# Performance work log

Measured on AMD Instinct MI355X. Metric: run time of the kernel, lower is better.

## Reference

```python
import jax, jax.numpy as jnp
import numpy as np

B, S, D, UNITS = 32, 4096, 512, 512


def setup_inputs() -> dict:
    key = jax.random.key(0)
    ks = jax.random.split(key, 8)
    scale = 0.05
    return {
        "query": jax.random.normal(ks[0], (B, D), dtype=jnp.float32),
        "values": jax.random.normal(ks[1], (B, S, D), dtype=jnp.float32),
        "W1": jax.random.normal(ks[2], (D, UNITS), dtype=jnp.float32) * scale,
        "b1": jnp.zeros((UNITS,), dtype=jnp.float32),
        "W2": jax.random.normal(ks[3], (D, UNITS), dtype=jnp.float32) * scale,
        "b2": jnp.zeros((UNITS,), dtype=jnp.float32),
        "V": jax.random.normal(ks[4], (UNITS, 1), dtype=jnp.float32) * scale,
        "bv": jnp.zeros((1,), dtype=jnp.float32),
    }


def reference(query, values, W1, b1, W2, b2, V, bv):
    # values: [B, S, D], query: [B, D]
    proj_v = jnp.einsum("bsd,du->bsu", values, W1) + b1          # [B, S, U]
    proj_q = (query @ W2 + b2)[:, None, :]                        # [B, 1, U]
    score = jnp.tanh(proj_v + proj_q) @ V + bv                    # [B, S, 1]
    attention_weights = jax.nn.softmax(score, axis=1)             # [B, S, 1]
    context_vector = jnp.sum(attention_weights * values, axis=1)  # [B, D]
    return (context_vector, attention_weights)
```

## Files before the change

### kernel.cpp

```cpp
#include <hip/hip_runtime.h>

#define NB 32
#define NS 4096
#define ND 512
#define NU 512

typedef __attribute__((ext_vector_type(8))) __bf16 bf16x8;
typedef __attribute__((ext_vector_type(8))) short short8;
typedef __attribute__((ext_vector_type(4))) float f32x4;

union Cvt8 { __bf16 h[8]; short8 s8; };

__device__ __forceinline__ float fast_tanh(float x) {
  float e = __expf(2.0f * x);
  return 1.0f - __fdividef(2.0f, e + 1.0f);
}

__global__ void pack_w1_kernel(const float* __restrict__ W1, __bf16* __restrict__ W1f) {
  int idx = blockIdx.x * 256 + threadIdx.x;
  int l  = idx & 63;
  int ct = (idx >> 6) & 31;
  int ks = idx >> 11;
  int col   = ct * 16 + (l & 15);
  int kbase = ks * 32 + (l >> 4) * 8;
  Cvt8 u;
#pragma unroll
  for (int j = 0; j < 8; ++j) u.h[j] = (__bf16)W1[(size_t)(kbase + j) * NU + col];
  *reinterpret_cast<short8*>(W1f + (size_t)idx * 8) = u.s8;
}

__global__ void proj_query_kernel(const float* __restrict__ query, const float* __restrict__ W2,
                                  const float* __restrict__ b2, const float* __restrict__ b1,
                                  float* __restrict__ pq) {
  int b = blockIdx.y;
  int u = blockIdx.x * 256 + threadIdx.x;
  const float* q = query + (size_t)b * ND;
  float acc = b2[u] + b1[u];
  for (int k = 0; k < ND; ++k) acc += q[k] * W2[(size_t)k * NU + u];
  pq[(size_t)b * NU + u] = acc;
}

__global__ __launch_bounds__(512, 4)
void score_kernel(const float* __restrict__ values, const __bf16* __restrict__ W1f,
                  const float* __restrict__ pq, const float* __restrict__ V,
                  float* __restrict__ scoreW) {
  __shared__ __align__(16) char ldsb[67584];
  float* sbuf = (float*)(ldsb + 65536);

  int bid = blockIdx.x;
  int b = bid >> 6;
  int s0 = (bid & 63) * 64;
  int tid = threadIdx.x;
  int l = tid & 63;
  int w = tid >> 6;
  int lane_col = l & 15;
  int lane_k8  = l >> 4;

  float pqv[4], Vv[4];
#pragma unroll
  for (int nb = 0; nb < 2; ++nb)
#pragma unroll
    for (int cf = 0; cf < 2; ++cf) {
      int col = nb * 256 + w * 32 + cf * 16 + lane_col;
      pqv[nb * 2 + cf] = pq[(size_t)b * NU + col];
      Vv[nb * 2 + cf]  = V[col];
    }

  const float* vbase = values + ((size_t)b * NS + s0) * ND;

#pragma unroll
  for (int i = 0; i < 8; ++i) {
    int c  = i * 512 + tid;
    int t  = c >> 10;
    int kg = (c >> 6) & 15;
    int ln = c & 63;
    int s  = t * 16 + (ln & 15);
    int c8 = kg * 4 + (ln >> 4);
    const float4* p = reinterpret_cast<const float4*>(vbase + (size_t)s * ND + c8 * 8);
    float4 f0 = p[0], f1 = p[1];
    Cvt8 u;
    u.h[0] = (__bf16)f0.x; u.h[1] = (__bf16)f0.y; u.h[2] = (__bf16)f0.z; u.h[3] = (__bf16)f0.w;
    u.h[4] = (__bf16)f1.x; u.h[5] = (__bf16)f1.y; u.h[6] = (__bf16)f1.z; u.h[7] = (__bf16)f1.w;
    *reinterpret_cast<short8*>(ldsb + (size_t)c * 16) = u.s8;
  }
  __syncthreads();

  float partial[4][4];
#pragma unroll
  for (int t = 0; t < 4; ++t)
#pragma unroll
    for (int r = 0; r < 4; ++r) partial[t][r] = 0.f;

#pragma unroll
  for (int nb = 0; nb < 2; ++nb) {
    f32x4 acc[4][2];
#pragma unroll
    for (int t = 0; t < 4; ++t)
#pragma unroll
      for (int cf = 0; cf < 2; ++cf) acc[t][cf] = (f32x4){0.f, 0.f, 0.f, 0.f};

    const __bf16* wp = W1f + ((size_t)(nb * 16 + w * 2) * 64 + l) * 8;

    for (int kg = 0; kg < 16; ++kg) {
      bf16x8 a[4];
#pragma unroll
      for (int t = 0; t < 4; ++t)
        a[t] = *reinterpret_cast<const bf16x8*>(ldsb + (((t * 16 + kg) * 64 + l) << 4));
      bf16x8 bb[2];
#pragma unroll
      for (int cf = 0; cf < 2; ++cf)
        bb[cf] = *reinterpret_cast<const bf16x8*>(wp + (size_t)kg * 16384 + cf * 512);
      __builtin_amdgcn_s_setprio(1);
#pragma unroll
      for (int cf = 0; cf < 2; ++cf)
#pragma unroll
        for (int t = 0; t < 4; ++t)
          acc[t][cf] = __builtin_amdgcn_mfma_f32_16x16x32_bf16(a[t], bb[cf], acc[t][cf], 0, 0, 0);
      __builtin_amdgcn_s_setprio(0);
    }

#pragma unroll
    for (int cf = 0; cf < 2; ++cf)
#pragma unroll
      for (int t = 0; t < 4; ++t)
#pragma unroll
        for (int r = 0; r < 4; ++r)
          partial[t][r] += fast_tanh(acc[t][cf][r] + pqv[nb * 2 + cf]) * Vv[nb * 2 + cf];
  }

#pragma unroll
  for (int off = 1; off < 16; off <<= 1)
#pragma unroll
    for (int t = 0; t < 4; ++t)
#pragma unroll
      for (int r = 0; r < 4; ++r) partial[t][r] += __shfl_xor(partial[t][r], off);

  if (lane_col == 0) {
#pragma unroll
    for (int t = 0; t < 4; ++t)
#pragma unroll
      for (int r = 0; r < 4; ++r)
        sbuf[w * 64 + t * 16 + lane_k8 * 4 + r] = partial[t][r];
  }
  __syncthreads();
  if (tid < 64) {
    float sc = 0.f;
#pragma unroll
    for (int wv = 0; wv < 8; ++wv) sc += sbuf[wv * 64 + tid];
    scoreW[(size_t)b * NS + s0 + tid] = sc;
  }
}

__global__ void softmax_kernel(const float* __restrict__ scoreW, float* __restrict__ attn) {
  int b = blockIdx.x, tid = threadIdx.x;
  __shared__ float sred[8];
  const float* sc = scoreW + (size_t)b * NS;
  float m = -3.0e38f;
  for (int s = tid; s < NS; s += 256) m = fmaxf(m, sc[s]);
#pragma unroll
  for (int off = 1; off < 64; off <<= 1) m = fmaxf(m, __shfl_xor(m, off));
  if ((tid & 63) == 0) sred[tid >> 6] = m;
  __syncthreads();
  m = fmaxf(fmaxf(sred[0], sred[1]), fmaxf(sred[2], sred[3]));
  float sum = 0.f;
  for (int s = tid; s < NS; s += 256) sum += __expf(sc[s] - m);
#pragma unroll
  for (int off = 1; off < 64; off <<= 1) sum += __shfl_xor(sum, off);
  if ((tid & 63) == 0) sred[4 + (tid >> 6)] = sum;
  __syncthreads();
  float inv = 1.f / (sred[4] + sred[5] + sred[6] + sred[7]);
  float* ab = attn + (size_t)b * NS;
  for (int s = tid; s < NS; s += 256) ab[s] = __expf(sc[s] - m) * inv;
}

__global__ void context_partial_kernel(const float* __restrict__ values,
                                       const float* __restrict__ attn,
                                       float* __restrict__ ctxpart) {
  int blk = blockIdx.x;
  int b = blk >> 4, c = blk & 15;
  int tid = threadIdx.x;
  int t2 = tid & 127;
  int sg = tid >> 7;
  const float* vb = values + ((size_t)b * NS + c * 256) * ND;
  const float* ab = attn + (size_t)b * NS + c * 256;
  f32x4 acc = {0.f, 0.f, 0.f, 0.f};
  for (int s = sg; s < 256; s += 2) {
    float wv = ab[s];
    f32x4 v = *reinterpret_cast<const f32x4*>(vb + (size_t)s * ND + t2 * 4);
    acc += v * wv;
  }
  __shared__ f32x4 red[128];
  if (sg == 1) red[t2] = acc;
  __syncthreads();
  if (sg == 0) {
    acc += red[t2];
    *reinterpret_cast<f32x4*>(ctxpart + (size_t)blk * ND + t2 * 4) = acc;
  }
}

__global__ void context_reduce_kernel(const float* __restrict__ ctxpart, float* __restrict__ ctx) {
  int b = blockIdx.x, tid = threadIdx.x;
  f32x4 acc = {0.f, 0.f, 0.f, 0.f};
  for (int c = 0; c < 16; ++c)
    acc += *reinterpret_cast<const f32x4*>(ctxpart + (size_t)(b * 16 + c) * ND + tid * 4);
  *reinterpret_cast<f32x4*>(ctx + (size_t)b * ND + tid * 4) = acc;
}

extern "C" void kernel_launch(void* const* d_in, const int* in_sizes, int n_in,
                              void* d_out, int out_size, void* d_ws, size_t ws_size,
                              hipStream_t stream) {
  const float* query  = (const float*)d_in[0];
  const float* values = (const float*)d_in[1];
  const float* W1     = (const float*)d_in[2];
  const float* b1     = (const float*)d_in[3];
  const float* W2     = (const float*)d_in[4];
  const float* b2     = (const float*)d_in[5];
  const float* V      = (const float*)d_in[6];

  float* ctx_out  = (float*)d_out;
  float* attn_out = ctx_out + NB * ND;

  char* ws = (char*)d_ws;
  __bf16* W1f    = (__bf16*)ws;
  float*  pq     = (float*)(ws + 524288);
  float*  scoreW = (float*)(ws + 589824);
  float*  ctxp   = (float*)(ws + 1114112);

  hipLaunchKernelGGL(pack_w1_kernel,        dim3(128),     dim3(256), 0, stream, W1, W1f);
  hipLaunchKernelGGL(proj_query_kernel,     dim3(2, NB),   dim3(256), 0, stream, query, W2, b2, b1, pq);
  hipLaunchKernelGGL(score_kernel,          dim3(2048),    dim3(512), 0, stream, values, W1f, pq, V, scoreW);
  hipLaunchKernelGGL(softmax_kernel,        dim3(NB),      dim3(256), 0, stream, scoreW, attn_out);
  hipLaunchKernelGGL(context_partial_kernel,dim3(NB * 16), dim3(256), 0, stream, values, attn_out, ctxp);
  hipLaunchKernelGGL(context_reduce_kernel, dim3(NB),      dim3(128), 0, stream, ctxp, ctx_out);
}
```

Before: 200.6 us.

## Stage W1 tiles into an LDS ring via async global-to-LDS loads

The score kernel's B operand (packed bf16 W1) is no longer read from global memory straight into registers on every k-step. It is now copied into a 4-slot LDS ring with `global_load_lds` DMA, three stages ahead, using a waitcnt plus barrier per step and a fully unrolled k loop. The aim is to hide W1 fetch latency behind the MFMAs and share each tile across the 8 waves of a block. In exchange, the block's LDS footprint roughly doubles, the launch bound drops to 2, and a barrier is added every k-step, which lowers occupancy. The fixed `vmcnt(4)` wait may not cover the last ring stages, so correctness at the tail depends on compiler-inserted waits.

```diff
diff --git a/kernel.cpp b/kernel.cpp
--- a/kernel.cpp
+++ b/kernel.cpp
@@ -14,6 +14,12 @@
 __device__ __forceinline__ float fast_tanh(float x) {
   float e = __expf(2.0f * x);
   return 1.0f - __fdividef(2.0f, e + 1.0f);
+}
+
+__device__ __forceinline__ void gload_lds16(const void* g, void* l) {
+  __builtin_amdgcn_global_load_lds(
+      (const __attribute__((address_space(1))) unsigned int*)g,
+      (__attribute__((address_space(3))) unsigned int*)l, 16, 0, 0);
 }
 
 __global__ void pack_w1_kernel(const float* __restrict__ W1, __bf16* __restrict__ W1f) {
@@ -40,12 +46,14 @@
   pq[(size_t)b * NU + u] = acc;
 }
 
-__global__ __launch_bounds__(512, 4)
+__global__ __launch_bounds__(512, 2)
 void score_kernel(const float* __restrict__ values, const __bf16* __restrict__ W1f,
                   const float* __restrict__ pq, const float* __restrict__ V,
                   float* __restrict__ scoreW) {
-  __shared__ __align__(16) char ldsb[67584];
-  float* sbuf = (float*)(ldsb + 65536);
+  __shared__ __align__(16) char ldsb[133120];
+  char* vtile = ldsb;
+  char* bring = ldsb + 65536;
+  float* sbuf = (float*)(ldsb + 131072);
 
   int bid = blockIdx.x;
   int b = bid >> 6;
@@ -66,8 +74,17 @@
       Vv[nb * 2 + cf]  = V[col];
     }
 
+  const char* wbase = (const char*)W1f;
+  auto stageB = [&](int j) {
+    int nb = j >> 4, ks = j & 15;
+    const char* src = wbase + ((size_t)(ks * 32 + nb * 16) << 10);
+    char* dst = bring + (j & 3) * 16384;
+    gload_lds16(src + tid * 16, dst + tid * 16);
+    gload_lds16(src + 8192 + tid * 16, dst + 8192 + tid * 16);
+  };
+
+  stageB(0); stageB(1); stageB(2);
   const float* vbase = values + ((size_t)b * NS + s0) * ND;
-
 #pragma unroll
   for (int i = 0; i < 8; ++i) {
     int c  = i * 512 + tid;
@@ -76,12 +93,12 @@
     int ln = c & 63;
     int s  = t * 16 + (ln & 15);
     int c8 = kg * 4 + (ln >> 4);
-    const float4* p = reinterpret_cast<const float4*>(vbase + (size_t)s * ND + c8 * 8);
-    float4 f0 = p[0], f1 = p[1];
+    const f32x4* p = reinterpret_cast<const f32x4*>(vbase + (size_t)s * ND + c8 * 8);
+    f32x4 f0 = p[0], f1 = p[1];
     Cvt8 u;
     u.h[0] = (__bf16)f0.x; u.h[1] = (__bf16)f0.y; u.h[2] = (__bf16)f0.z; u.h[3] = (__bf16)f0.w;
     u.h[4] = (__bf16)f1.x; u.h[5] = (__bf16)f1.y; u.h[6] = (__bf16)f1.z; u.h[7] = (__bf16)f1.w;
-    *reinterpret_cast<short8*>(ldsb + (size_t)c * 16) = u.s8;
+    *reinterpret_cast<short8*>(vtile + (size_t)c * 16) = u.s8;
   }
   __syncthreads();
 
@@ -99,24 +116,25 @@
 #pragma unroll
       for (int cf = 0; cf < 2; ++cf) acc[t][cf] = (f32x4){0.f, 0.f, 0.f, 0.f};
 
-    const __bf16* wp = W1f + ((size_t)(nb * 16 + w * 2) * 64 + l) * 8;
-
-    for (int kg = 0; kg < 16; ++kg) {
-      bf16x8 a[4];
+#pragma unroll
+    for (int ks = 0; ks < 16; ++ks) {
+      const int kg = nb * 16 + ks;
+      asm volatile("s_waitcnt vmcnt(4)" ::: "memory");
+      __builtin_amdgcn_s_barrier();
+      char* slot = bring + (kg & 3) * 16384;
+      bf16x8 a[4], bb[2];
 #pragma unroll
       for (int t = 0; t < 4; ++t)
-        a[t] = *reinterpret_cast<const bf16x8*>(ldsb + (((t * 16 + kg) * 64 + l) << 4));
-      bf16x8 bb[2];
+        a[t] = *reinterpret_cast<const bf16x8*>(vtile + (((t * 16 + ks) * 64 + l) << 4));
 #pragma unroll
       for (int cf = 0; cf < 2; ++cf)
-        bb[cf] = *reinterpret_cast<const bf16x8*>(wp + (size_t)kg * 16384 + cf * 512);
-      __builtin_amdgcn_s_setprio(1);
+        bb[cf] = *reinterpret_cast<const bf16x8*>(slot + ((w * 2 + cf) << 10) + (l << 4));
 #pragma unroll
       for (int cf = 0; cf < 2; ++cf)
 #pragma unroll
         for (int t = 0; t < 4; ++t)
           acc[t][cf] = __builtin_amdgcn_mfma_f32_16x16x32_bf16(a[t], bb[cf], acc[t][cf], 0, 0, 0);
-      __builtin_amdgcn_s_setprio(0);
+      if (kg + 3 < 32) stageB(kg + 3);
     }
 
 #pragma unroll
```

Measured after the change: 223.6 us. +11.5%, slower.
